# Kernel tuning notes

Hardware: AMD Instinct MI355X
Metric: run time of the kernel (lower is better)

The kernel has to match this reference:

```python
import jax, jax.numpy as jnp
import numpy as np

NUM_HEADS = 16
ROPE_BASE = 10000.0


def _rope_interleaved(x, cos, sin):
    # x: (B, S, H, hd); cos/sin: (1, S, 1, hd//2)
    x1 = x[..., ::2]
    x2 = x[..., 1::2]
    r1 = x1 * cos - x2 * sin
    r2 = x1 * sin + x2 * cos
    return jnp.stack([r1, r2], axis=-1).reshape(x.shape)


def _rope_tables(seq_len, head_dim, dtype):
    dim = head_dim // 2
    freqs = jnp.exp(-jnp.arange(0, dim, dtype=dtype) * jnp.log(jnp.asarray(ROPE_BASE, dtype)) / dim)
    pos = jnp.arange(seq_len, dtype=dtype)
    angles = pos[:, None] * freqs[None, :]  # (S, hd//2)
    return jnp.cos(angles)[None, :, None, :], jnp.sin(angles)[None, :, None, :]


def setup_inputs() -> dict:
    key = jax.random.key(0)
    ks = jax.random.split(key, 9)
    B, S, D = 2, 2048, 2048
    sc = 1.0 / np.sqrt(D)
    return {
        "x": jax.random.normal(ks[0], (B, S, D), jnp.float32),
        "wq": jax.random.normal(ks[1], (D, D), jnp.float32) * sc,
        "bq": jax.random.normal(ks[2], (D,), jnp.float32) * 0.01,
        "wk": jax.random.normal(ks[3], (D, D), jnp.float32) * sc,
        "bk": jax.random.normal(ks[4], (D,), jnp.float32) * 0.01,
        "wv": jax.random.normal(ks[5], (D, D), jnp.float32) * sc,
        "bv": jax.random.normal(ks[6], (D,), jnp.float32) * 0.01,
        "wo": jax.random.normal(ks[7], (D, D), jnp.float32) * sc,
        "bo": jax.random.normal(ks[8], (D,), jnp.float32) * 0.01,
    }


def reference(x, wq, bq, wk, bk, wv, bv, wo, bo):
    B, S, D = x.shape
    H = NUM_HEADS
    hd = D // H
    # QKV projections (eqx.nn.Linear: y = W @ x + b, weight (out, in))
    q = (x @ wq.T + bq).reshape(B, S, H, hd)
    k = (x @ wk.T + bk).reshape(B, S, H, hd)
    v = (x @ wv.T + bv).reshape(B, S, H, hd)
    # RoPE (interleaved / GPT-NeoX style)
    cos, sin = _rope_tables(S, hd, x.dtype)
    q = _rope_interleaved(q, cos, sin)
    k = _rope_interleaved(k, cos, sin)
    # Causal scaled dot-product attention
    scale = 1.0 / np.sqrt(hd)
    scores = jnp.einsum("bqhd,bkhd->bhqk", q, k) * scale
    causal = jnp.tril(jnp.ones((S, S), dtype=bool))
    scores = jnp.where(causal[None, None, :, :], scores, jnp.finfo(scores.dtype).min)
    attn = jax.nn.softmax(scores, axis=-1)
    out = jnp.einsum("bhqk,bkhd->bqhd", attn, v).reshape(B, S, D)
    return out @ wo.T + bo
```

## Files before the change

### kernel.cpp

```cpp
#include <hip/hip_runtime.h>

typedef unsigned short u16;
typedef short bf16x8 __attribute__((ext_vector_type(8)));
typedef float f32x4 __attribute__((ext_vector_type(4)));

#define B_ 2
#define S_ 2048
#define D_ 2048
#define HD_ 128
#define GW 512
#define KB 64
#define VST 72
#define PST 72

__device__ __forceinline__ float bf2f(u16 h) {
  unsigned u = ((unsigned)h) << 16;
  return __builtin_bit_cast(float, u);
}
__device__ __forceinline__ u16 f2bf(float f) {
  unsigned u = __builtin_bit_cast(unsigned, f);
  u += 0x7FFF + ((u >> 16) & 1);
  return (u16)(u >> 16);
}
__device__ __forceinline__ bf16x8 cvt8(const float* p) {
  float4 a = *(const float4*)p;
  float4 b = *(const float4*)(p + 4);
  bf16x8 r;
  r[0] = (short)f2bf(a.x); r[1] = (short)f2bf(a.y);
  r[2] = (short)f2bf(a.z); r[3] = (short)f2bf(a.w);
  r[4] = (short)f2bf(b.x); r[5] = (short)f2bf(b.y);
  r[6] = (short)f2bf(b.z); r[7] = (short)f2bf(b.w);
  return r;
}

__device__ __forceinline__ void gload16(const void* g, void* lds) {
  __builtin_amdgcn_global_load_lds(
      (const __attribute__((address_space(1))) unsigned*)g,
      (__attribute__((address_space(3))) unsigned*)lds, 16, 0, 0);
}

__device__ __forceinline__ f32x4 mfma16(bf16x8 a, bf16x8 b, f32x4 c) {
  return __builtin_amdgcn_mfma_f32_16x16x32_bf16(a, b, c, 0, 0, 0);
}

__global__ void k_cvt_all(const float* __restrict__ x, const float* __restrict__ wq,
                          const float* __restrict__ wk, const float* __restrict__ wv,
                          const float* __restrict__ wo, u16* __restrict__ xb,
                          u16* __restrict__ wqkvb, u16* wob, float2* tab) {
  const int slice = blockIdx.y;
  const int i = blockIdx.x * 256 + threadIdx.x;
  if (slice == 5) {
    if (tab != nullptr && i < 131072) {
      const int s = i >> 6, ip = i & 63;
      const float freq = expf(-(float)ip * 0.14391157f);
      float sv, cv;
      sincosf((float)s * freq, &sv, &cv);
      tab[i] = make_float2(cv, sv);
    }
    return;
  }
  if (slice == 4 && wob == nullptr) return;
  const float* src;
  u16* dst;
  int n8;
  if (slice == 0) { src = x; dst = xb; n8 = 1048576; }
  else if (slice == 1) { src = wq; dst = wqkvb; n8 = 524288; }
  else if (slice == 2) { src = wk; dst = wqkvb + 4194304; n8 = 524288; }
  else if (slice == 3) { src = wv; dst = wqkvb + 8388608; n8 = 524288; }
  else { src = wo; dst = wob; n8 = 524288; }
  if (i < n8) *(bf16x8*)(dst + (size_t)i * 8) = cvt8(src + (size_t)i * 8);
}

template <int AM, int WM, int CM>
__device__ __forceinline__ void gemm_body(const void* Ap, const void* Wp,
                                          const float* __restrict__ bias,
                                          void* Cp, int ldc,
                                          const float2* __restrict__ tab) {
  constexpr int K = 2048;
  __shared__ u16 As[128 * 32];
  __shared__ u16 Bs[128 * 32];
  const int t = threadIdx.x;
  const int w = t >> 6, l = t & 63, lr = l & 15, lg = l >> 4;
  const int m0 = blockIdx.y * 128, n0 = blockIdx.x * 128;
  const int wr = w >> 1, wc = w & 1;

  f32x4 acc[4][4];
#pragma unroll
  for (int i = 0; i < 4; ++i)
#pragma unroll
    for (int j = 0; j < 4; ++j) acc[i][j] = f32x4{0.f, 0.f, 0.f, 0.f};

  const int rowA0 = t >> 2, ko0 = (t & 3) * 8;
  const int rowA1 = (t + 256) >> 2, ko1 = ((t + 256) & 3) * 8;

  for (int kt = 0; kt < K; kt += 32) {
    if constexpr (AM == 1) {
      const u16* A = (const u16*)Ap;
      gload16(A + (size_t)(m0 + rowA0) * K + kt + ko0, (char*)As + (size_t)w * 1024);
      gload16(A + (size_t)(m0 + rowA1) * K + kt + ko1, (char*)As + (size_t)(w + 4) * 1024);
    } else {
      const float* A = (const float*)Ap;
      *(bf16x8*)((char*)As + (size_t)t * 16) = cvt8(A + (size_t)(m0 + rowA0) * K + kt + ko0);
      *(bf16x8*)((char*)As + (size_t)(t + 256) * 16) = cvt8(A + (size_t)(m0 + rowA1) * K + kt + ko1);
    }
    if constexpr (WM == 1) {
      const u16* W = (const u16*)Wp;
      gload16(W + (size_t)(n0 + rowA0) * K + kt + ko0, (char*)Bs + (size_t)w * 1024);
      gload16(W + (size_t)(n0 + rowA1) * K + kt + ko1, (char*)Bs + (size_t)(w + 4) * 1024);
    } else {
      const float* W = (const float*)Wp;
      *(bf16x8*)((char*)Bs + (size_t)t * 16) = cvt8(W + (size_t)(n0 + rowA0) * K + kt + ko0);
      *(bf16x8*)((char*)Bs + (size_t)(t + 256) * 16) = cvt8(W + (size_t)(n0 + rowA1) * K + kt + ko1);
    }
    __syncthreads();

    bf16x8 af[4], bw[4];
#pragma unroll
    for (int i = 0; i < 4; ++i) {
      af[i] = *(const bf16x8*)(As + (size_t)(wr * 64 + i * 16 + lr) * 32 + lg * 8);
      bw[i] = *(const bf16x8*)(Bs + (size_t)(wc * 64 + i * 16 + lr) * 32 + lg * 8);
    }
#pragma unroll
    for (int i = 0; i < 4; ++i)
#pragma unroll
      for (int j = 0; j < 4; ++j)
        acc[i][j] = mfma16(af[i], bw[j], acc[i][j]);
    __syncthreads();
  }

#pragma unroll
  for (int i = 0; i < 4; ++i) {
#pragma unroll
    for (int j = 0; j < 4; ++j) {
      const int col = n0 + wc * 64 + j * 16 + lr;
      const float bv = bias[col];
      const int row = m0 + wr * 64 + i * 16 + lg * 4;
      if (CM == 0 && tab != nullptr) {
        const int ip = (col & 127) >> 1;
        const int odd = col & 1;
#pragma unroll
        for (int r = 0; r < 4; ++r) {
          const float v = acc[i][j][r] + bv;
          const float p = __shfl_xor(v, 1, 64);
          const float2 cs = tab[((row + r) & (S_ - 1)) * 64 + ip];
          const float o = odd ? (p * cs.y + v * cs.x) : (v * cs.x - p * cs.y);
          ((u16*)Cp)[(size_t)(row + r) * ldc + col] = f2bf(o);
        }
      } else {
#pragma unroll
        for (int r = 0; r < 4; ++r) {
          if constexpr (CM == 1)
            ((float*)Cp)[(size_t)(row + r) * ldc + col] = acc[i][j][r] + bv;
          else
            ((u16*)Cp)[(size_t)(row + r) * ldc + col] = f2bf(acc[i][j][r] + bv);
        }
      }
    }
  }
}

__global__ __launch_bounds__(256) void k_gemm_qkv_bb(
    const u16* __restrict__ xb, const u16* __restrict__ wqkvb,
    const float* __restrict__ bq, const float* __restrict__ bk,
    const float* __restrict__ bv, u16* __restrict__ q, u16* __restrict__ k,
    u16* __restrict__ v, const float2* __restrict__ tab) {
  const int z = blockIdx.z;
  const u16* W = wqkvb + (size_t)z * D_ * D_;
  const float* bias = z == 0 ? bq : (z == 1 ? bk : bv);
  u16* C = z == 0 ? q : (z == 1 ? k : v);
  gemm_body<1, 1, 0>(xb, W, bias, C, D_, z == 2 ? nullptr : tab);
}

__global__ __launch_bounds__(256) void k_gemm_out_bb(
    const u16* __restrict__ ao, const u16* __restrict__ wob,
    const float* __restrict__ bo, float* __restrict__ out) {
  gemm_body<1, 1, 1>(ao, wob, bo, out, D_, nullptr);
}

__global__ __launch_bounds__(256) void k_gemm_qkv_xb(
    const u16* __restrict__ xb, const float* __restrict__ wq,
    const float* __restrict__ bq, const float* __restrict__ wk,
    const float* __restrict__ bk, const float* __restrict__ wv,
    const float* __restrict__ bv, u16* __restrict__ q, u16* __restrict__ k,
    u16* __restrict__ v) {
  const int z = blockIdx.z;
  const float* W = z == 0 ? wq : (z == 1 ? wk : wv);
  const float* bias = z == 0 ? bq : (z == 1 ? bk : bv);
  u16* C = z == 0 ? q : (z == 1 ? k : v);
  gemm_body<1, 0, 0>(xb, W, bias, C, D_, nullptr);
}

__global__ __launch_bounds__(256) void k_gemm_out(const u16* __restrict__ ao,
                                                  const float* __restrict__ wo,
                                                  const float* __restrict__ bo,
                                                  float* __restrict__ out) {
  gemm_body<1, 0, 1>(ao, wo, bo, out, D_, nullptr);
}

__global__ __launch_bounds__(256) void k_gemm_qkv_g(
    const float* __restrict__ x, const float* __restrict__ wq,
    const float* __restrict__ bq, const float* __restrict__ wk,
    const float* __restrict__ bk, const float* __restrict__ wv,
    const float* __restrict__ bv, u16* __restrict__ qg, u16* __restrict__ kg,
    u16* __restrict__ vg, int g) {
  const int z = blockIdx.z;
  const float* W = (z == 0 ? wq : (z == 1 ? wk : wv)) + (size_t)g * GW * D_;
  const float* bias = (z == 0 ? bq : (z == 1 ? bk : bv)) + g * GW;
  u16* C = z == 0 ? qg : (z == 1 ? kg : vg);
  gemm_body<0, 0, 0>(x, W, bias, C, GW, nullptr);
}

__device__ __forceinline__ void rope_one(u16* p, float cv, float sv) {
  unsigned u = *(const unsigned*)p;
  float x1 = bf2f((u16)(u & 0xffff)), x2 = bf2f((u16)(u >> 16));
  unsigned r = (unsigned)f2bf(x1 * cv - x2 * sv) |
               ((unsigned)f2bf(x1 * sv + x2 * cv) << 16);
  *(unsigned*)p = r;
}

__global__ void k_rope_full(u16* q, u16* kk) {
  const int idx = blockIdx.x * 256 + threadIdx.x;
  const int i = idx & 63;
  const int hh = (idx >> 6) & 15;
  const int bs = idx >> 10;
  const int s = bs & (S_ - 1);
  const float freq = expf(-(float)i * 0.14391157f);
  float sv, cv;
  sincosf((float)s * freq, &sv, &cv);
  const size_t off = (size_t)bs * D_ + (size_t)hh * HD_ + 2 * i;
  rope_one(q + off, cv, sv);
  rope_one(kk + off, cv, sv);
}

__global__ void k_rope_g(u16* q, u16* kk) {
  const int idx = blockIdx.x * 256 + threadIdx.x;
  const int i = idx & 63;
  const int hh = (idx >> 6) & 3;
  const int bs = idx >> 8;
  const int s = bs & (S_ - 1);
  const float freq = expf(-(float)i * 0.14391157f);
  float sv, cv;
  sincosf((float)s * freq, &sv, &cv);
  const size_t off = (size_t)bs * GW + (size_t)hh * HD_ + 2 * i;
  rope_one(q + off, cv, sv);
  rope_one(kk + off, cv, sv);
}

__device__ __forceinline__ void attn_body(const u16* Q, const u16* Kd,
                                          const u16* V, u16* O,
                                          size_t base_in, size_t base_out,
                                          int ld_in, int ld_out, int q0) {
  const int t = threadIdx.x, w = t >> 6, l = t & 63, lr = l & 15, lg = l >> 4;

  __shared__ u16 Ks[2][KB * HD_];
  __shared__ u16 Vt[2][HD_ * VST];
  __shared__ u16 Ps[4][16 * PST];

  bf16x8 qf[4];
  {
    const u16* qp = Q + base_in + (size_t)(q0 + w * 16 + lr) * ld_in;
#pragma unroll
    for (int ds = 0; ds < 4; ++ds)
      qf[ds] = *(const bf16x8*)(qp + ds * 32 + lg * 8);
  }

  f32x4 oacc[8];
#pragma unroll
  for (int f = 0; f < 8; ++f) oacc[f] = f32x4{0.f, 0.f, 0.f, 0.f};
  float mrow = -1e30f, lrow = 0.f;

  const int qrow = q0 + w * 16 + lr;
  const int nt = q0 / KB + 1;
  const float sc = 0.08838834764831845f;

  const int c1 = t + 256;
  const int kk20 = (t & 31) * 2, d00 = (t >> 5) * 8;
  const int kk21 = (c1 & 31) * 2, d01 = (c1 >> 5) * 8;

  bf16x8 vc[4];

#pragma unroll
  for (int r = 0; r < 4; ++r) {
    const int c = t + 256 * r;
    const int row = c >> 4, c16 = c & 15;
    const int gc = c16 ^ (row & 7);
    gload16(Kd + base_in + (size_t)row * ld_in + gc * 8,
            (char*)Ks[0] + (size_t)(w + 4 * r) * 1024);
  }
  vc[0] = *(const bf16x8*)(V + base_in + (size_t)kk20 * ld_in + d00);
  vc[1] = *(const bf16x8*)(V + base_in + (size_t)(kk20 + 1) * ld_in + d00);
  vc[2] = *(const bf16x8*)(V + base_in + (size_t)kk21 * ld_in + d01);
  vc[3] = *(const bf16x8*)(V + base_in + (size_t)(kk21 + 1) * ld_in + d01);

  for (int tt = 0; tt < nt; ++tt) {
    const int cur = tt & 1;
    const int kv0 = tt * KB;
    const bool more = (tt + 1 < nt);

    if (more) {
      const int kvn = kv0 + KB;
#pragma unroll
      for (int r = 0; r < 4; ++r) {
        const int c = t + 256 * r;
        const int row = c >> 4, c16 = c & 15;
        const int gc = c16 ^ (row & 7);
        gload16(Kd + base_in + (size_t)(kvn + row) * ld_in + gc * 8,
                (char*)Ks[cur ^ 1] + (size_t)(w + 4 * r) * 1024);
      }
      asm volatile("s_waitcnt vmcnt(4)" ::: "memory");
    } else {
      asm volatile("s_waitcnt vmcnt(0)" ::: "memory");
    }
    __builtin_amdgcn_sched_barrier(0);

    {
      u16* vt = Vt[cur];
#pragma unroll
      for (int j = 0; j < 8; ++j) {
        unsigned p0 = (unsigned)(unsigned short)vc[0][j] |
                      ((unsigned)(unsigned short)vc[1][j] << 16);
        *(unsigned*)&vt[(size_t)(d00 + j) * VST + kk20] = p0;
        unsigned p1 = (unsigned)(unsigned short)vc[2][j] |
                      ((unsigned)(unsigned short)vc[3][j] << 16);
        *(unsigned*)&vt[(size_t)(d01 + j) * VST + kk21] = p1;
      }
    }
    if (more) {
      const int kvn = kv0 + KB;
      vc[0] = *(const bf16x8*)(V + base_in + (size_t)(kvn + kk20) * ld_in + d00);
      vc[1] = *(const bf16x8*)(V + base_in + (size_t)(kvn + kk20 + 1) * ld_in + d00);
      vc[2] = *(const bf16x8*)(V + base_in + (size_t)(kvn + kk21) * ld_in + d01);
      vc[3] = *(const bf16x8*)(V + base_in + (size_t)(kvn + kk21 + 1) * ld_in + d01);
    }
    asm volatile("s_waitcnt lgkmcnt(0)" ::: "memory");
    __builtin_amdgcn_sched_barrier(0);
    __builtin_amdgcn_s_barrier();
    __builtin_amdgcn_sched_barrier(0);

    float p[16];
    __builtin_amdgcn_s_setprio(1);
#pragma unroll
    for (int h = 0; h < 4; ++h) {
      f32x4 s = {0.f, 0.f, 0.f, 0.f};
#pragma unroll
      for (int ds = 0; ds < 4; ++ds) {
        const int ch = (ds * 4 + lg) ^ (lr & 7);
        bf16x8 kf = *(const bf16x8*)(Ks[cur] + (size_t)(h * 16 + lr) * HD_ + ch * 8);
        s = mfma16(kf, qf[ds], s);
      }
#pragma unroll
      for (int r = 0; r < 4; ++r) p[h * 4 + r] = s[r] * sc;
    }
    __builtin_amdgcn_s_setprio(0);
    if (kv0 + KB - 1 > q0 + w * 16) {
#pragma unroll
      for (int h = 0; h < 4; ++h)
#pragma unroll
        for (int r = 0; r < 4; ++r)
          if (kv0 + h * 16 + lg * 4 + r > qrow) p[h * 4 + r] = -1e30f;
    }
    float pm = p[0];
#pragma unroll
    for (int i = 1; i < 16; ++i) pm = fmaxf(pm, p[i]);
    pm = fmaxf(pm, __shfl_xor(pm, 16, 64));
    pm = fmaxf(pm, __shfl_xor(pm, 32, 64));
    const float mn = fmaxf(mrow, pm);
    const float scl = __expf(mrow - mn);
    mrow = mn;
    float rs = 0.f;
#pragma unroll
    for (int i = 0; i < 16; ++i) {
      p[i] = __expf(p[i] - mn);
      rs += p[i];
    }
    rs += __shfl_xor(rs, 16, 64);
    rs += __shfl_xor(rs, 32, 64);
    lrow = lrow * scl + rs;
    float sj[4];
#pragma unroll
    for (int j = 0; j < 4; ++j) sj[j] = __shfl(scl, lg * 4 + j, 64);
#pragma unroll
    for (int f = 0; f < 8; ++f)
#pragma unroll
      for (int j = 0; j < 4; ++j) oacc[f][j] *= sj[j];
#pragma unroll
    for (int h = 0; h < 4; ++h)
#pragma unroll
      for (int r = 0; r < 4; ++r)
        Ps[w][lr * PST + h * 16 + lg * 4 + r] = f2bf(p[h * 4 + r]);
    bf16x8 pf0 = *(const bf16x8*)&Ps[w][lr * PST + lg * 8];
    bf16x8 pf1 = *(const bf16x8*)&Ps[w][lr * PST + 32 + lg * 8];
    __builtin_amdgcn_s_setprio(1);
#pragma unroll
    for (int f = 0; f < 8; ++f) {
      bf16x8 vf0 = *(const bf16x8*)&Vt[cur][(size_t)(f * 16 + lr) * VST + lg * 8];
      bf16x8 vf1 = *(const bf16x8*)&Vt[cur][(size_t)(f * 16 + lr) * VST + 32 + lg * 8];
      oacc[f] = mfma16(pf0, vf0, oacc[f]);
      oacc[f] = mfma16(pf1, vf1, oacc[f]);
    }
    __builtin_amdgcn_s_setprio(0);
    __builtin_amdgcn_sched_barrier(0);
    __builtin_amdgcn_s_barrier();
    __builtin_amdgcn_sched_barrier(0);
  }

  const float inv = 1.0f / lrow;
  float ij[4];
#pragma unroll
  for (int j = 0; j < 4; ++j) ij[j] = __shfl(inv, lg * 4 + j, 64);
  u16* Op = O + base_out;
#pragma unroll
  for (int f = 0; f < 8; ++f)
#pragma unroll
    for (int j = 0; j < 4; ++j)
      Op[(size_t)(q0 + w * 16 + lg * 4 + j) * ld_out + f * 16 + lr] =
          f2bf(oacc[f][j] * ij[j]);
}

#define TILE_COMPUTE(QT, QROW, QF, MROW, LROW, OACC)                           \
  {                                                                            \
    float p[16];                                                               \
    __builtin_amdgcn_s_setprio(1);                                             \
    _Pragma("unroll") for (int h = 0; h < 4; ++h) {                            \
      f32x4 s = {0.f, 0.f, 0.f, 0.f};                                          \
      _Pragma("unroll") for (int ds = 0; ds < 4; ++ds) {                       \
        const int ch = (ds * 4 + lg) ^ (lr & 7);                               \
        bf16x8 kf = *(const bf16x8*)(Ks[cur] +                                 \
                                     (size_t)(h * 16 + lr) * HD_ + ch * 8);    \
        s = mfma16(kf, QF[ds], s);                                             \
      }                                                                        \
      _Pragma("unroll") for (int r = 0; r < 4; ++r) p[h * 4 + r] = s[r] * sc;  \
    }                                                                          \
    __builtin_amdgcn_s_setprio(0);                                             \
    if (kv0 + KB - 1 > (QT) + w * 16) {                                        \
      _Pragma("unroll") for (int h = 0; h < 4; ++h)                            \
          _Pragma("unroll") for (int r = 0; r < 4; ++r) if (kv0 + h * 16 +     \
                                                            lg * 4 + r >      \
                                                            (QROW))           \
              p[h * 4 + r] = -1e30f;                                           \
    }                                                                          \
    float pm = p[0];                                                           \
    _Pragma("unroll") for (int i = 1; i < 16; ++i) pm = fmaxf(pm, p[i]);       \
    pm = fmaxf(pm, __shfl_xor(pm, 16, 64));                                    \
    pm = fmaxf(pm, __shfl_xor(pm, 32, 64));                                    \
    if (!__all(pm <= (MROW) + 8.f)) {                                          \
      const float mn = fmaxf(MROW, pm);                                        \
      const float scl = __expf((MROW)-mn);                                     \
      MROW = mn;                                                               \
      float sj[4];                                                             \
      _Pragma("unroll") for (int j = 0; j < 4; ++j) sj[j] =                    \
          __shfl(scl, lg * 4 + j, 64);                                         \
      _Pragma("unroll") for (int f = 0; f < 8; ++f)                            \
          _Pragma("unroll") for (int j = 0; j < 4; ++j) OACC[f][j] *= sj[j];   \
      LROW *= scl;                                                             \
    }                                                                          \
    float rs = 0.f;                                                            \
    _Pragma("unroll") for (int i = 0; i < 16; ++i) {                           \
      p[i] = __expf(p[i] - (MROW));                                            \
      rs += p[i];                                                              \
    }                                                                          \
    rs += __shfl_xor(rs, 16, 64);                                              \
    rs += __shfl_xor(rs, 32, 64);                                              \
    LROW += rs;                                                                \
    _Pragma("unroll") for (int h = 0; h < 4; ++h)                              \
        _Pragma("unroll") for (int r = 0; r < 4; ++r)                          \
            Ps[w][lr * PST + h * 16 + lg * 4 + r] = f2bf(p[h * 4 + r]);        \
    bf16x8 pf0 = *(const bf16x8*)&Ps[w][lr * PST + lg * 8];                    \
    bf16x8 pf1 = *(const bf16x8*)&Ps[w][lr * PST + 32 + lg * 8];               \
    __builtin_amdgcn_s_setprio(1);                                             \
    _Pragma("unroll") for (int f = 0; f < 8; ++f) {                            \
      bf16x8 vf0 =                                                             \
          *(const bf16x8*)&Vt[cur][(size_t)(f * 16 + lr) * VST + lg * 8];      \
      bf16x8 vf1 =                                                             \
          *(const bf16x8*)&Vt[cur][(size_t)(f * 16 + lr) * VST + 32 + lg * 8]; \
      OACC[f] = mfma16(pf0, vf0, OACC[f]);                                     \
      OACC[f] = mfma16(pf1, vf1, OACC[f]);                                     \
    }                                                                          \
    __builtin_amdgcn_s_setprio(0);                                             \
  }

__global__ __launch_bounds__(256) void k_attn_full(const u16* Q, const u16* Kd,
                                                   const u16* V, u16* O) {
  const int lin = blockIdx.y * gridDim.x + blockIdx.x;
  const int work = (lin & 7) * 64 + (lin >> 3);
  const int bh = work >> 4;
  const int pr = work & 15;
  const int b = bh >> 4, h = bh & 15;
  const size_t base = ((size_t)b * S_) * D_ + (size_t)h * HD_;
  const int qA = 64 * (31 - pr), qB = 64 * pr;

  const int t = threadIdx.x, w = t >> 6, l = t & 63, lr = l & 15, lg = l >> 4;

  __shared__ u16 Ks[2][KB * HD_];
  __shared__ u16 Vt[2][HD_ * VST];
  __shared__ u16 Ps[4][16 * PST];

  bf16x8 qfA[4], qfB[4];
  {
    const u16* qp = Q + base + (size_t)(qA + w * 16 + lr) * D_;
#pragma unroll
    for (int ds = 0; ds < 4; ++ds)
      qfA[ds] = *(const bf16x8*)(qp + ds * 32 + lg * 8);
    qp = Q + base + (size_t)(qB + w * 16 + lr) * D_;
#pragma unroll
    for (int ds = 0; ds < 4; ++ds)
      qfB[ds] = *(const bf16x8*)(qp + ds * 32 + lg * 8);
  }

  f32x4 oaccA[8], oaccB[8];
#pragma unroll
  for (int f = 0; f < 8; ++f) {
    oaccA[f] = f32x4{0.f, 0.f, 0.f, 0.f};
    oaccB[f] = f32x4{0.f, 0.f, 0.f, 0.f};
  }
  float mrowA = -1e30f, lrowA = 0.f, mrowB = -1e30f, lrowB = 0.f;
  const int qrowA = qA + w * 16 + lr, qrowB = qB + w * 16 + lr;
  const int ntA = qA / KB + 1;
  const float sc = 0.08838834764831845f;

  const int c1 = t + 256;
  const int kk20 = (t & 31) * 2, d00 = (t >> 5) * 8;
  const int kk21 = (c1 & 31) * 2, d01 = (c1 >> 5) * 8;

  bf16x8 vc[4];

#pragma unroll
  for (int r = 0; r < 4; ++r) {
    const int c = t + 256 * r;
    const int row = c >> 4, c16 = c & 15;
    const int gc = c16 ^ (row & 7);
    gload16(Kd + base + (size_t)row * D_ + gc * 8,
            (char*)Ks[0] + (size_t)(w + 4 * r) * 1024);
  }
  vc[0] = *(const bf16x8*)(V + base + (size_t)kk20 * D_ + d00);
  vc[1] = *(const bf16x8*)(V + base + (size_t)(kk20 + 1) * D_ + d00);
  vc[2] = *(const bf16x8*)(V + base + (size_t)kk21 * D_ + d01);
  vc[3] = *(const bf16x8*)(V + base + (size_t)(kk21 + 1) * D_ + d01);

  for (int tt = 0; tt < ntA; ++tt) {
    const int cur = tt & 1;
    const int kv0 = tt * KB;
    const bool more = (tt + 1 < ntA);

    if (more) {
      const int kvn = kv0 + KB;
#pragma unroll
      for (int r = 0; r < 4; ++r) {
        const int c = t + 256 * r;
        const int row = c >> 4, c16 = c & 15;
        const int gc = c16 ^ (row & 7);
        gload16(Kd + base + (size_t)(kvn + row) * D_ + gc * 8,
                (char*)Ks[cur ^ 1] + (size_t)(w + 4 * r) * 1024);
      }
      asm volatile("s_waitcnt vmcnt(4)" ::: "memory");
    } else {
      asm volatile("s_waitcnt vmcnt(0)" ::: "memory");
    }
    __builtin_amdgcn_sched_barrier(0);

    {
      u16* vt = Vt[cur];
#pragma unroll
      for (int j = 0; j < 8; ++j) {
        unsigned p0 = (unsigned)(unsigned short)vc[0][j] |
                      ((unsigned)(unsigned short)vc[1][j] << 16);
        *(unsigned*)&vt[(size_t)(d00 + j) * VST + kk20] = p0;
        unsigned p1 = (unsigned)(unsigned short)vc[2][j] |
                      ((unsigned)(unsigned short)vc[3][j] << 16);
        *(unsigned*)&vt[(size_t)(d01 + j) * VST + kk21] = p1;
      }
    }
    if (more) {
      const int kvn = kv0 + KB;
      vc[0] = *(const bf16x8*)(V + base + (size_t)(kvn + kk20) * D_ + d00);
      vc[1] = *(const bf16x8*)(V + base + (size_t)(kvn + kk20 + 1) * D_ + d00);
      vc[2] = *(const bf16x8*)(V + base + (size_t)(kvn + kk21) * D_ + d01);
      vc[3] = *(const bf16x8*)(V + base + (size_t)(kvn + kk21 + 1) * D_ + d01);
    }
    asm volatile("s_waitcnt lgkmcnt(0)" ::: "memory");
    __builtin_amdgcn_sched_barrier(0);
    __builtin_amdgcn_s_barrier();
    __builtin_amdgcn_sched_barrier(0);

    TILE_COMPUTE(qA, qrowA, qfA, mrowA, lrowA, oaccA);
    if (tt <= pr) {
      TILE_COMPUTE(qB, qrowB, qfB, mrowB, lrowB, oaccB);
    }

    __builtin_amdgcn_sched_barrier(0);
    __builtin_amdgcn_s_barrier();
    __builtin_amdgcn_sched_barrier(0);
  }

  {
    const float inv = 1.0f / lrowA;
    float ij[4];
#pragma unroll
    for (int j = 0; j < 4; ++j) ij[j] = __shfl(inv, lg * 4 + j, 64);
    u16* Op = O + base;
#pragma unroll
    for (int f = 0; f < 8; ++f)
#pragma unroll
      for (int j = 0; j < 4; ++j)
        Op[(size_t)(qA + w * 16 + lg * 4 + j) * D_ + f * 16 + lr] =
            f2bf(oaccA[f][j] * ij[j]);
  }
  {
    const float inv = 1.0f / lrowB;
    float ij[4];
#pragma unroll
    for (int j = 0; j < 4; ++j) ij[j] = __shfl(inv, lg * 4 + j, 64);
    u16* Op = O + base;
#pragma unroll
    for (int f = 0; f < 8; ++f)
#pragma unroll
      for (int j = 0; j < 4; ++j)
        Op[(size_t)(qB + w * 16 + lg * 4 + j) * D_ + f * 16 + lr] =
            f2bf(oaccB[f][j] * ij[j]);
  }
}
#undef TILE_COMPUTE

__global__ __launch_bounds__(256) void k_attn_g(const u16* __restrict__ Q,
                                                const u16* __restrict__ Kd,
                                                const u16* __restrict__ V,
                                                u16* __restrict__ O, int g) {
  const int by = blockIdx.y;
  const int b = by >> 2, hh = by & 3;
  const size_t base_in = ((size_t)b * S_) * GW + (size_t)hh * HD_;
  const size_t base_out = ((size_t)b * S_) * D_ + (size_t)(g * 4 + hh) * HD_;
  attn_body(Q, Kd, V, O, base_in, base_out, GW, D_, blockIdx.x * 64);
}

extern "C" void kernel_launch(void* const* d_in, const int* in_sizes, int n_in,
                              void* d_out, int out_size, void* d_ws,
                              size_t ws_size, hipStream_t stream) {
  (void)in_sizes; (void)n_in; (void)out_size;
  const float* x = (const float*)d_in[0];
  const float* wq = (const float*)d_in[1];
  const float* bq = (const float*)d_in[2];
  const float* wk = (const float*)d_in[3];
  const float* bk = (const float*)d_in[4];
  const float* wv = (const float*)d_in[5];
  const float* bv = (const float*)d_in[6];
  const float* wo = (const float*)d_in[7];
  const float* bo = (const float*)d_in[8];
  float* out = (float*)d_out;

  const size_t XB = (size_t)B_ * S_ * D_ * 2;
  const size_t WB3 = 3 * (size_t)D_ * D_ * 2;
  const size_t WB1 = (size_t)D_ * D_ * 2;
  const size_t TB = (size_t)S_ * 64 * 8;
  char* ws = (char*)d_ws;
  char* ob = (char*)d_out;

  u16 *xb, *q, *k, *v, *wqkvb = nullptr, *wob = nullptr;
  float2* tab = nullptr;
  int tier;
  if (ws_size >= 4 * XB + WB3 + WB1 + TB) {
    xb = (u16*)ws; q = (u16*)(ws + XB); k = (u16*)(ws + 2 * XB);
    v = (u16*)(ws + 3 * XB);
    wqkvb = (u16*)(ws + 4 * XB); wob = (u16*)(ws + 4 * XB + WB3);
    tab = (float2*)(ws + 4 * XB + WB3 + WB1);
    tier = 1;
  } else if (ws_size >= 3 * XB + WB3 + WB1 + TB) {
    xb = (u16*)ob;
    q = (u16*)ws; k = (u16*)(ws + XB); v = (u16*)(ws + 2 * XB);
    wqkvb = (u16*)(ws + 3 * XB); wob = (u16*)(ws + 3 * XB + WB3);
    tab = (float2*)(ws + 3 * XB + WB3 + WB1);
    tier = 1;
  } else if (ws_size >= 2 * XB + WB3 + TB) {
    xb = (u16*)ob; v = (u16*)(ob + XB);
    q = (u16*)ws; k = (u16*)(ws + XB);
    wqkvb = (u16*)(ws + 2 * XB);
    tab = (float2*)(ws + 2 * XB + WB3);
    tier = 2;
  } else if (ws_size >= 2 * XB) {
    xb = (u16*)ob; v = (u16*)(ob + XB);
    q = (u16*)ws; k = (u16*)(ws + XB);
    tier = 3;
  } else {
    tier = 4;
  }

  if (tier == 1 || tier == 2) {
    dim3 gc(4096, 6);
    k_cvt_all<<<gc, 256, 0, stream>>>(x, wq, wk, wv, wo, xb, wqkvb, wob, tab);
    dim3 g1(16, 32, 3);
    k_gemm_qkv_bb<<<g1, 256, 0, stream>>>(xb, wqkvb, bq, bk, bv, q, k, v, tab);
    dim3 g2(16, 32);
    k_attn_full<<<g2, 256, 0, stream>>>(q, k, v, q);
    dim3 g3(16, 32);
    if (tier == 1)
      k_gemm_out_bb<<<g3, 256, 0, stream>>>(q, wob, bo, out);
    else
      k_gemm_out<<<g3, 256, 0, stream>>>(q, wo, bo, out);
  } else if (tier == 3) {
    dim3 gc(4096, 1);
    k_cvt_all<<<gc, 256, 0, stream>>>(x, wq, wk, wv, wo, xb, xb, nullptr, nullptr);
    dim3 g1(16, 32, 3);
    k_gemm_qkv_xb<<<g1, 256, 0, stream>>>(xb, wq, bq, wk, bk, wv, bv, q, k, v);
    k_rope_full<<<16384, 256, 0, stream>>>(q, k);
    dim3 g2(16, 32);
    k_attn_full<<<g2, 256, 0, stream>>>(q, k, v, q);
    dim3 g3(16, 32);
    k_gemm_out<<<g3, 256, 0, stream>>>(q, wo, bo, out);
  } else {
    u16* qg = (u16*)ob;
    u16* kg = qg + (size_t)(B_ * S_) * GW;
    u16* vg = kg + (size_t)(B_ * S_) * GW;
    u16* ao = (u16*)ws;
    for (int g = 0; g < 4; ++g) {
      dim3 g1(4, 32, 3);
      k_gemm_qkv_g<<<g1, 256, 0, stream>>>(x, wq, bq, wk, bk, wv, bv, qg, kg, vg, g);
      k_rope_g<<<4096, 256, 0, stream>>>(qg, kg);
      dim3 g2(32, 8);
      k_attn_g<<<g2, 256, 0, stream>>>(qg, kg, vg, ao, g);
    }
    dim3 g3(16, 32);
    k_gemm_out<<<g3, 256, 0, stream>>>(ao, wo, bo, out);
  }
}
```

Measured before the change: 276.6 us.

## Remap GEMM tiles across XCDs and flatten conversion grid to drop idle blocks

GEMM kernels now remap the linear block index so that consecutive tiles dispatched round-robin to the same XCD cover contiguous row/column regions. This is meant to improve L2 reuse of A and W tiles per die. The conversion kernel uses a flat 1D grid sized to the actual work instead of a 4096x6 grid, so blocks that previously exited early with no work are no longer launched. The remap assumes a 16x32 grid and 8 XCDs.

New measurement: 272.3 us (median of 2 runs). About the same (-1.5%).

```diff
diff --git a/kernel.cpp b/kernel.cpp
--- a/kernel.cpp
+++ b/kernel.cpp
@@ -47,10 +47,10 @@
                           const float* __restrict__ wk, const float* __restrict__ wv,
                           const float* __restrict__ wo, u16* __restrict__ xb,
                           u16* __restrict__ wqkvb, u16* wob, float2* tab) {
-  const int slice = blockIdx.y;
-  const int i = blockIdx.x * 256 + threadIdx.x;
-  if (slice == 5) {
-    if (tab != nullptr && i < 131072) {
+  const int bx = blockIdx.x;
+  if (bx >= 12288) {
+    if (tab != nullptr) {
+      const int i = (bx - 12288) * 256 + threadIdx.x;
       const int s = i >> 6, ip = i & 63;
       const float freq = expf(-(float)ip * 0.14391157f);
       float sv, cv;
@@ -59,29 +59,38 @@
     }
     return;
   }
-  if (slice == 4 && wob == nullptr) return;
   const float* src;
   u16* dst;
-  int n8;
-  if (slice == 0) { src = x; dst = xb; n8 = 1048576; }
-  else if (slice == 1) { src = wq; dst = wqkvb; n8 = 524288; }
-  else if (slice == 2) { src = wk; dst = wqkvb + 4194304; n8 = 524288; }
-  else if (slice == 3) { src = wv; dst = wqkvb + 8388608; n8 = 524288; }
-  else { src = wo; dst = wob; n8 = 524288; }
-  if (i < n8) *(bf16x8*)(dst + (size_t)i * 8) = cvt8(src + (size_t)i * 8);
+  int i;
+  if (bx < 4096) { src = x; dst = xb; i = bx * 256 + threadIdx.x; }
+  else if (bx < 6144) { src = wq; dst = wqkvb; i = (bx - 4096) * 256 + threadIdx.x; }
+  else if (bx < 8192) { src = wk; dst = wqkvb + 4194304; i = (bx - 6144) * 256 + threadIdx.x; }
+  else if (bx < 10240) { src = wv; dst = wqkvb + 8388608; i = (bx - 8192) * 256 + threadIdx.x; }
+  else {
+    if (wob == nullptr) return;
+    src = wo; dst = wob; i = (bx - 10240) * 256 + threadIdx.x;
+  }
+  *(bf16x8*)(dst + (size_t)i * 8) = cvt8(src + (size_t)i * 8);
+}
+
+__device__ __forceinline__ void xcd_remap512(int& m0, int& n0) {
+  const int lin = blockIdx.y * 16 + blockIdx.x;
+  const int wk = (lin & 7) * 64 + (lin >> 3);
+  m0 = (wk >> 4) * 128;
+  n0 = (wk & 15) * 128;
 }
 
 template <int AM, int WM, int CM>
 __device__ __forceinline__ void gemm_body(const void* Ap, const void* Wp,
                                           const float* __restrict__ bias,
                                           void* Cp, int ldc,
-                                          const float2* __restrict__ tab) {
+                                          const float2* __restrict__ tab,
+                                          int m0, int n0) {
   constexpr int K = 2048;
   __shared__ u16 As[128 * 32];
   __shared__ u16 Bs[128 * 32];
   const int t = threadIdx.x;
   const int w = t >> 6, l = t & 63, lr = l & 15, lg = l >> 4;
-  const int m0 = blockIdx.y * 128, n0 = blockIdx.x * 128;
   const int wr = w >> 1, wc = w & 1;
 
   f32x4 acc[4][4];
@@ -168,13 +177,17 @@
   const u16* W = wqkvb + (size_t)z * D_ * D_;
   const float* bias = z == 0 ? bq : (z == 1 ? bk : bv);
   u16* C = z == 0 ? q : (z == 1 ? k : v);
-  gemm_body<1, 1, 0>(xb, W, bias, C, D_, z == 2 ? nullptr : tab);
+  int m0, n0;
+  xcd_remap512(m0, n0);
+  gemm_body<1, 1, 0>(xb, W, bias, C, D_, z == 2 ? nullptr : tab, m0, n0);
 }
 
 __global__ __launch_bounds__(256) void k_gemm_out_bb(
     const u16* __restrict__ ao, const u16* __restrict__ wob,
     const float* __restrict__ bo, float* __restrict__ out) {
-  gemm_body<1, 1, 1>(ao, wob, bo, out, D_, nullptr);
+  int m0, n0;
+  xcd_remap512(m0, n0);
+  gemm_body<1, 1, 1>(ao, wob, bo, out, D_, nullptr, m0, n0);
 }
 
 __global__ __launch_bounds__(256) void k_gemm_qkv_xb(
@@ -187,14 +200,18 @@
   const float* W = z == 0 ? wq : (z == 1 ? wk : wv);
   const float* bias = z == 0 ? bq : (z == 1 ? bk : bv);
   u16* C = z == 0 ? q : (z == 1 ? k : v);
-  gemm_body<1, 0, 0>(xb, W, bias, C, D_, nullptr);
+  int m0, n0;
+  xcd_remap512(m0, n0);
+  gemm_body<1, 0, 0>(xb, W, bias, C, D_, nullptr, m0, n0);
 }
 
 __global__ __launch_bounds__(256) void k_gemm_out(const u16* __restrict__ ao,
                                                   const float* __restrict__ wo,
                                                   const float* __restrict__ bo,
                                                   float* __restrict__ out) {
-  gemm_body<1, 0, 1>(ao, wo, bo, out, D_, nullptr);
+  int m0, n0;
+  xcd_remap512(m0, n0);
+  gemm_body<1, 0, 1>(ao, wo, bo, out, D_, nullptr, m0, n0);
 }
 
 __global__ __launch_bounds__(256) void k_gemm_qkv_g(
@@ -207,7 +224,8 @@
   const float* W = (z == 0 ? wq : (z == 1 ? wk : wv)) + (size_t)g * GW * D_;
   const float* bias = (z == 0 ? bq : (z == 1 ? bk : bv)) + g * GW;
   u16* C = z == 0 ? qg : (z == 1 ? kg : vg);
-  gemm_body<0, 0, 0>(x, W, bias, C, GW, nullptr);
+  gemm_body<0, 0, 0>(x, W, bias, C, GW, nullptr, blockIdx.y * 128,
+                     blockIdx.x * 128);
 }
 
 __device__ __forceinline__ void rope_one(u16* p, float cv, float sv) {
@@ -684,8 +702,7 @@
   }
 
   if (tier == 1 || tier == 2) {
-    dim3 gc(4096, 6);
-    k_cvt_all<<<gc, 256, 0, stream>>>(x, wq, wk, wv, wo, xb, wqkvb, wob, tab);
+    k_cvt_all<<<12800, 256, 0, stream>>>(x, wq, wk, wv, wo, xb, wqkvb, wob, tab);
     dim3 g1(16, 32, 3);
     k_gemm_qkv_bb<<<g1, 256, 0, stream>>>(xb, wqkvb, bq, bk, bv, q, k, v, tab);
     dim3 g2(16, 32);
@@ -696,8 +713,7 @@
     else
       k_gemm_out<<<g3, 256, 0, stream>>>(q, wo, bo, out);
   } else if (tier == 3) {
-    dim3 gc(4096, 1);
-    k_cvt_all<<<gc, 256, 0, stream>>>(x, wq, wk, wv, wo, xb, xb, nullptr, nullptr);
+    k_cvt_all<<<4096, 256, 0, stream>>>(x, wq, wk, wv, wo, xb, xb, nullptr, nullptr);
     dim3 g1(16, 32, 3);
     k_gemm_qkv_xb<<<g1, 256, 0, stream>>>(xb, wq, bq, wk, bk, wv, bv, q, k, v);
     k_rope_full<<<16384, 256, 0, stream>>>(q, k);
```
